# Performance work log

Measured on AMD Instinct MI355X. Metric: run time of the kernel, lower is better.

Reference implementation:

```python
import jax, jax.numpy as jnp
import numpy as np
import math
from jax import lax

PI4 = math.pi / 4.0
BN_EPS = 1e-5


def rotate_kernel(kernel, angle):
    """Bilinear-interpolated rotation of a [Cg, Cg, k, k] kernel by scalar angle."""
    k = kernel.shape[-1]
    c = (k - 1) / 2.0
    cos_t = jnp.cos(angle)
    sin_t = jnp.sin(angle)
    y = jnp.arange(k, dtype=kernel.dtype) - c
    yy, xx = jnp.meshgrid(y, y, indexing='ij')
    x_rot = xx * cos_t + yy * sin_t + c
    y_rot = -xx * sin_t + yy * cos_t + c
    x0 = jnp.clip(jnp.floor(x_rot), 0, k - 2)
    y0 = jnp.clip(jnp.floor(y_rot), 0, k - 2)
    x1 = x0 + 1.0
    y1 = y0 + 1.0
    w00 = (x1 - x_rot) * (y1 - y_rot)
    w01 = (x1 - x_rot) * (y_rot - y0)
    w10 = (x_rot - x0) * (y1 - y_rot)
    w11 = (x_rot - x0) * (y_rot - y0)
    x0i = x0.astype(jnp.int32)
    y0i = y0.astype(jnp.int32)
    x1i = x1.astype(jnp.int32)
    y1i = y1.astype(jnp.int32)
    g = lambda yi, xi: kernel[:, :, yi, xi]  # advanced index -> [Cg,Cg,k,k]
    return w00 * g(y0i, x0i) + w01 * g(y1i, x0i) + w10 * g(y0i, x1i) + w11 * g(y1i, x1i)


def bn_inf(x, w, b, m, v):
    scale = (w / jnp.sqrt(v + BN_EPS))[None, :, None, None]
    return (x - m[None, :, None, None]) * scale + b[None, :, None, None]


def resize_bilinear_ac(x, Ho, Wo):
    """Bilinear resize, align_corners=True, x: [B,C,H,W]."""
    B, C, H, W = x.shape
    ys = jnp.linspace(0.0, H - 1.0, Ho)
    xs = jnp.linspace(0.0, W - 1.0, Wo)
    y0 = jnp.clip(jnp.floor(ys), 0, H - 2).astype(jnp.int32)
    x0 = jnp.clip(jnp.floor(xs), 0, W - 2).astype(jnp.int32)
    wy = (ys - y0)[:, None]
    wx = (xs - x0)[None, :]
    yi0 = y0[:, None]
    xi0 = x0[None, :]
    v00 = x[:, :, yi0, xi0]
    v01 = x[:, :, yi0, xi0 + 1]
    v10 = x[:, :, yi0 + 1, xi0]
    v11 = x[:, :, yi0 + 1, xi0 + 1]
    return (v00 * (1 - wy) * (1 - wx) + v01 * (1 - wy) * wx
            + v10 * wy * (1 - wx) + v11 * wy * wx)


def dac(x, base_kernel, aw1, ab1, aw2, ab2, mw1, mb1, mw2, mb2):
    B, C, H, W = x.shape
    G, Cg = base_kernel.shape[0], base_kernel.shape[1]
    k = base_kernel.shape[-1]
    pad = (k - 1) // 2
    pooled = x.mean(axis=(2, 3))  # [B,C]  (AdaptiveAvgPool2d(1))
    h = jax.nn.relu(pooled @ aw1.T + ab1)
    angles = jnp.tanh(h @ aw2.T + ab2) * PI4  # [B,G]
    # rotate per-(batch, group) kernels: [B,G,Cg,Cg,k,k]
    rot = jax.vmap(lambda ang_b: jax.vmap(rotate_kernel)(base_kernel, ang_b))(angles)
    rhs = rot.reshape(B * C, Cg, k, k)
    # per-sample grouped conv folded into one conv with B*G groups
    feat = lax.conv_general_dilated(
        x.reshape(1, B * C, H, W), rhs, (1, 1), ((pad, pad), (pad, pad)),
        dimension_numbers=('NCHW', 'OIHW', 'NCHW'),
        feature_group_count=B * G).reshape(B, C, H, W)
    mod = jax.nn.sigmoid(jax.nn.relu(pooled @ mw1.T + mb1) @ mw2.T + mb2)  # [B,C]
    return feat * mod[:, :, None, None]


def setup_inputs() -> dict:
    key = jax.random.key(0)
    ks = jax.random.split(key, 32)
    B, C, H, W = 8, 64, 128, 128
    G, Cg, K = 8, 8, 3
    hid = C // 4  # angle/meta hidden = 16
    Ch = C // 2   # edge hidden = 32
    n = lambda i, shape, s: jax.random.normal(ks[i], shape, jnp.float32) * s
    d = {}
    d['x'] = jax.random.normal(ks[0], (B, C, H, W), jnp.float32)
    d['roi_mask'] = jax.random.uniform(ks[1], (B, 1, H // 2, W // 2), jnp.float32)
    # 4 DAC branches stacked on leading axis
    d['base_kernel'] = n(2, (4, G, Cg, Cg, K, K), 0.17)  # kaiming fan_out std
    d['ang_w1'] = n(3, (4, hid, C), 0.1); d['ang_b1'] = n(4, (4, hid), 0.1)
    d['ang_w2'] = n(5, (4, G, hid), 0.1); d['ang_b2'] = n(6, (4, G), 0.1)
    d['meta_w1'] = n(7, (4, hid, C), 0.1); d['meta_b1'] = n(8, (4, hid), 0.1)
    d['meta_w2'] = n(9, (4, C, hid), 0.1); d['meta_b2'] = n(10, (4, C), 0.1)
    # dir_attn: Conv2d_BN(4C->C) + ReLU + Conv(C->4) + Softmax
    d['dir_w1'] = n(11, (C, 4 * C), 0.05)
    d['dir_bn_w'] = jnp.ones((C,), jnp.float32)
    d['dir_bn_b'] = jnp.zeros((C,), jnp.float32)
    d['dir_bn_m'] = n(12, (C,), 0.01)
    d['dir_bn_v'] = jax.random.uniform(ks[13], (C,), jnp.float32, 0.5, 1.5)
    d['dir_w2'] = n(14, (4, C), 0.1); d['dir_b2'] = n(15, (4,), 0.1)
    # edge_attn: Conv2d_BN(C->C/2) + ReLU + Conv(C/2->C) + Sigmoid
    d['edge_w1'] = n(16, (Ch, C), 0.1)
    d['edge_bn_w'] = jnp.ones((Ch,), jnp.float32)
    d['edge_bn_b'] = jnp.zeros((Ch,), jnp.float32)
    d['edge_bn_m'] = n(17, (Ch,), 0.01)
    d['edge_bn_v'] = jax.random.uniform(ks[18], (Ch,), jnp.float32, 0.5, 1.5)
    d['edge_w2'] = n(19, (C, Ch), 0.1); d['edge_b2'] = n(20, (C,), 0.1)
    return d


def reference(x, roi_mask, base_kernel, ang_w1, ang_b1, ang_w2, ang_b2,
              meta_w1, meta_b1, meta_w2, meta_b2,
              dir_w1, dir_bn_w, dir_bn_b, dir_bn_m, dir_bn_v, dir_w2, dir_b2,
              edge_w1, edge_bn_w, edge_bn_b, edge_bn_m, edge_bn_v, edge_w2, edge_b2):
    branch_feats = [
        dac(x, base_kernel[i], ang_w1[i], ang_b1[i], ang_w2[i], ang_b2[i],
            meta_w1[i], meta_b1[i], meta_w2[i], meta_b2[i])
        for i in range(4)
    ]
    feats_cat = jnp.concatenate(branch_feats, axis=1)  # [B,4C,H,W]
    y = jnp.einsum('oc,bchw->bohw', dir_w1, feats_cat)
    y = jax.nn.relu(bn_inf(y, dir_bn_w, dir_bn_b, dir_bn_m, dir_bn_v))
    logits = jnp.einsum('oc,bchw->bohw', dir_w2, y) + dir_b2[None, :, None, None]
    attn = jax.nn.softmax(logits, axis=1)  # [B,4,H,W]
    fused = sum(branch_feats[i] * attn[:, i:i + 1] for i in range(4))
    B, C, H, W = fused.shape
    roi = resize_bilinear_ac(roi_mask, H, W)
    e = jnp.einsum('oc,bchw->bohw', edge_w1, fused * roi)
    e = jax.nn.relu(bn_inf(e, edge_bn_w, edge_bn_b, edge_bn_m, edge_bn_v))
    e = jax.nn.sigmoid(jnp.einsum('oc,bchw->bohw', edge_w2, e) + edge_b2[None, :, None, None])
    return x + x * e
```

## Files before the change

### kernel.cpp

```cpp
#include <hip/hip_runtime.h>
#include <hip/hip_bf16.h>
#include <math.h>

#define PI4F 0.78539816339744830962f

typedef __attribute__((ext_vector_type(2))) __bf16 bf16x2_t;
typedef __attribute__((ext_vector_type(8))) short s8v;
typedef __attribute__((ext_vector_type(4))) float f32x4;
typedef __attribute__((ext_vector_type(4))) unsigned int uint4v;

__device__ __forceinline__ float dot2bf(unsigned int a, unsigned int b, float c) {
#if defined(__has_builtin) && __has_builtin(__builtin_amdgcn_fdot2_f32_bf16)
    return __builtin_amdgcn_fdot2_f32_bf16(__builtin_bit_cast(bf16x2_t, a),
                                           __builtin_bit_cast(bf16x2_t, b), c, false);
#else
    float a0 = __uint_as_float(a << 16), a1 = __uint_as_float(a & 0xffff0000u);
    float b0 = __uint_as_float(b << 16), b1 = __uint_as_float(b & 0xffff0000u);
    return fmaf(a1, b1, fmaf(a0, b0, c));
#endif
}

__device__ __forceinline__ unsigned short bf16bits(float v) {
    return __builtin_bit_cast(unsigned short, __float2bfloat16(v));
}
__device__ __forceinline__ unsigned int packbf(float lo, float hi) {
    return (unsigned int)bf16bits(lo) | ((unsigned int)bf16bits(hi) << 16);
}
__device__ __forceinline__ float ubf_lo(unsigned int u) { return __uint_as_float(u << 16); }
__device__ __forceinline__ float ubf_hi(unsigned int u) { return __uint_as_float(u & 0xffff0000u); }

__global__ void k_pool(const float* __restrict__ x, float* __restrict__ pooled) {
    int bc = blockIdx.x;
    const float4* p4 = (const float4*)(x + (size_t)bc * 16384);
    float s = 0.f;
    for (int j = threadIdx.x; j < 4096; j += 256) {
        float4 v = p4[j];
        s += (v.x + v.y) + (v.z + v.w);
    }
    for (int off = 32; off > 0; off >>= 1) s += __shfl_xor(s, off, 64);
    __shared__ float red[4];
    int wave = threadIdx.x >> 6;
    if ((threadIdx.x & 63) == 0) red[wave] = s;
    __syncthreads();
    if (threadIdx.x == 0) {
        float t = red[0] + red[1] + red[2] + red[3];
        pooled[bc] = t * (1.0f / 16384.0f);
    }
}

__global__ void k_mlp(const float* __restrict__ pooled,
                      const float* __restrict__ aw1, const float* __restrict__ ab1,
                      const float* __restrict__ aw2, const float* __restrict__ ab2,
                      const float* __restrict__ mw1, const float* __restrict__ mb1,
                      const float* __restrict__ mw2, const float* __restrict__ mb2,
                      float* __restrict__ angles, float* __restrict__ mod) {
    int i = blockIdx.x >> 3, b = blockIdx.x & 7;
    int t = threadIdx.x;
    __shared__ float sp[64], sha[16], shm[16];
    sp[t] = pooled[b * 64 + t];
    __syncthreads();
    if (t < 16) {
        float sa = ab1[i * 16 + t], sm = mb1[i * 16 + t];
        const float* wa = aw1 + ((size_t)i * 16 + t) * 64;
        const float* wm = mw1 + ((size_t)i * 16 + t) * 64;
        for (int c = 0; c < 64; ++c) { sa = fmaf(wa[c], sp[c], sa); sm = fmaf(wm[c], sp[c], sm); }
        sha[t] = fmaxf(sa, 0.f);
        shm[t] = fmaxf(sm, 0.f);
    }
    __syncthreads();
    if (t < 8) {
        float s = ab2[i * 8 + t];
        const float* w = aw2 + ((size_t)i * 8 + t) * 16;
        for (int j = 0; j < 16; ++j) s = fmaf(w[j], sha[j], s);
        angles[i * 64 + b * 8 + t] = tanhf(s) * PI4F;
    }
    {
        float s = mb2[i * 64 + t];
        const float* w = mw2 + ((size_t)i * 64 + t) * 16;
        for (int j = 0; j < 16; ++j) s = fmaf(w[j], shm[j], s);
        mod[i * 512 + b * 64 + t] = 1.f / (1.f + expf(-s));
    }
}

__global__ void k_rot(const float* __restrict__ bk, const float* __restrict__ angles,
                      unsigned int* __restrict__ rotp) {
    int blk = blockIdx.x;
    int g = blk & 7, b = (blk >> 3) & 7, i = blk >> 6;
    float ang = angles[i * 64 + b * 8 + g];
    float st, ct;
    sincosf(ang, &st, &ct);
    int t = threadIdx.x;
    int co = t >> 3, ci = t & 7;
    const float* K = bk + ((((size_t)i * 8 + g) * 8 + co) * 8 + ci) * 9;
    __shared__ float tmp[576];
#pragma unroll
    for (int p = 0; p < 9; ++p) {
        int ky = p / 3, kx = p % 3;
        float xx = (float)kx - 1.f, yy = (float)ky - 1.f;
        float xr = xx * ct + yy * st + 1.f;
        float yr = -xx * st + yy * ct + 1.f;
        float x0 = fminf(fmaxf(floorf(xr), 0.f), 1.f);
        float y0 = fminf(fmaxf(floorf(yr), 0.f), 1.f);
        float x1 = x0 + 1.f, y1 = y0 + 1.f;
        float w00 = (x1 - xr) * (y1 - yr);
        float w01 = (x1 - xr) * (yr - y0);
        float w10 = (xr - x0) * (y1 - yr);
        float w11 = (xr - x0) * (yr - y0);
        int x0i = (int)x0, y0i = (int)y0;
        float v = w00 * K[y0i * 3 + x0i] + w01 * K[(y0i + 1) * 3 + x0i]
                + w10 * K[y0i * 3 + x0i + 1] + w11 * K[(y0i + 1) * 3 + x0i + 1];
        tmp[t * 9 + p] = v;
    }
    __syncthreads();
    unsigned int* R = rotp + (size_t)blk * 384;
    for (int ot = t; ot < 384; ot += 64) {
        int co2 = ot / 48;
        int rem = ot - co2 * 48;
        int tap = rem >> 2;
        int q = rem & 3;
        unsigned int val = 0u;
        if (tap < 9) {
            float v0 = tmp[(co2 * 8 + 2 * q) * 9 + tap];
            float v1 = tmp[(co2 * 8 + 2 * q + 1) * 9 + tap];
            val = packbf(v0, v1);
        }
        R[ot] = val;
    }
}

__global__ void k_prep(const float* __restrict__ w1,
                       const float* __restrict__ bnw, const float* __restrict__ bnb,
                       const float* __restrict__ bnm, const float* __restrict__ bnv,
                       const float* __restrict__ ew1,
                       const float* __restrict__ ebnw, const float* __restrict__ ebnb,
                       const float* __restrict__ ebnm, const float* __restrict__ ebnv,
                       const float* __restrict__ ew2,
                       unsigned int* __restrict__ w1f, float* __restrict__ dsh,
                       unsigned int* __restrict__ e1f, float* __restrict__ esh,
                       unsigned int* __restrict__ ew2p) {
    int tid = threadIdx.x;
    __shared__ float sc[64], sce[32];
    if (tid < 64) {
        float s = bnw[tid] * rsqrtf(bnv[tid] + 1e-5f);
        sc[tid] = s;
        dsh[tid] = bnb[tid] - bnm[tid] * s;
    }
    if (tid < 32) {
        float s = ebnw[tid] * rsqrtf(ebnv[tid] + 1e-5f);
        sce[tid] = s;
        esh[tid] = ebnb[tid] - ebnm[tid] * s;
    }
    __syncthreads();
    for (int q = tid; q < 8192; q += 256) {
        int jp = q & 3;
        int l  = (q >> 2) & 63;
        int ks = (q >> 8) & 7;
        int nt = q >> 11;
        int o = nt * 16 + (l & 15);
        int k = ks * 32 + (l >> 4) * 8 + jp * 2;
        w1f[q] = packbf(w1[o * 256 + k] * sc[o], w1[o * 256 + k + 1] * sc[o]);
    }
    for (int q = tid; q < 4096; q += 256) {
        int jp = q & 3;
        int l  = (q >> 2) & 63;
        int kss = (q >> 8) & 1;
        int nt8 = q >> 9;
        int o = (nt8 & 1) * 16 + (l & 15);
        int kloc = kss * 32 + (l >> 4) * 8 + jp * 2;
        e1f[q] = packbf(ew1[o * 64 + kloc] * sce[o], ew1[o * 64 + kloc + 1] * sce[o]);
    }
    for (int q = tid; q < 1024; q += 256) {
        int cc = q >> 4, c2 = q & 15;
        ew2p[q] = packbf(ew2[cc * 32 + 2 * c2], ew2[cc * 32 + 2 * c2 + 1]);
    }
}

__global__ void __launch_bounds__(256) k_conv(const float* __restrict__ x,
                       const unsigned int* __restrict__ rotp, const float* __restrict__ mod,
                       unsigned int* __restrict__ bfu) {
    __shared__ unsigned int s_in[1156 * 6];
    unsigned short* s16 = (unsigned short*)s_in;

    int bg = blockIdx.y;
    int b = bg >> 3, g = bg & 7;
    int tile_h0 = (blockIdx.x >> 2) * 32;
    int tile_w0 = (blockIdx.x & 3) * 32;
    int tid = threadIdx.x;

    const float* xg = x + ((size_t)b * 64 + (size_t)g * 8) * 16384;
    for (int idx = tid; idx < 8 * 1156; idx += 256) {
        int ci = idx / 1156;
        int pix = idx - ci * 1156;
        int r = pix / 34;
        int c = pix - r * 34;
        int gh = tile_h0 + r - 1;
        int gw = tile_w0 + c - 1;
        float v = 0.f;
        if (gh >= 0 && gh < 128 && gw >= 0 && gw < 128)
            v = xg[(size_t)ci * 16384 + gh * 128 + gw];
        s16[pix * 12 + ci] = bf16bits(v);
    }
    __syncthreads();

    int l = tid & 63, wv = tid >> 6;
    int n = l & 15;
    int kg = l >> 4;

    s8v Bf[2][3];
    float mv[2];
#pragma unroll
    for (int bp = 0; bp < 2; ++bp) {
        int i = bp * 2 + (n >> 3);
        int co = n & 7;
        mv[bp] = mod[i * 512 + b * 64 + g * 8 + co];
#pragma unroll
        for (int ks = 0; ks < 3; ++ks) {
            int tap = ks * 4 + kg;
            const uint4v* src = (const uint4v*)(rotp
                + ((size_t)((i * 8 + b) * 8 + g)) * 384 + co * 48 + tap * 4);
            Bf[bp][ks] = __builtin_bit_cast(s8v, *src);
        }
    }

    int hoff6[3];
#pragma unroll
    for (int ks = 0; ks < 3; ++ks) {
        int tap = ks * 4 + kg;
        int t9 = tap > 8 ? 8 : tap;
        int ky = t9 >= 6 ? 2 : (t9 >= 3 ? 1 : 0);
        int kx = t9 - ky * 3;
        hoff6[ks] = (ky * 34 + kx) * 6;
    }

#pragma unroll 2
    for (int t = 0; t < 16; ++t) {
        int px0 = wv * 256 + t * 16;
        int trow = px0 >> 5;
        int tcolb = px0 & 31;
        int basedw = (trow * 34 + tcolb + n) * 6;

        s8v Af[3];
#pragma unroll
        for (int ks = 0; ks < 3; ++ks) {
            const uint2* pa = (const uint2*)(s_in + basedw + hoff6[ks]);
            uint2 v01 = pa[0];
            uint2 v23 = pa[1];
            uint4v au; au.x = v01.x; au.y = v01.y; au.z = v23.x; au.w = v23.y;
            Af[ks] = __builtin_bit_cast(s8v, au);
        }

#pragma unroll
        for (int bp = 0; bp < 2; ++bp) {
            f32x4 acc = (f32x4){0.f, 0.f, 0.f, 0.f};
#pragma unroll
            for (int ks = 0; ks < 3; ++ks)
                acc = __builtin_amdgcn_mfma_f32_16x16x32_bf16(Af[ks], Bf[bp][ks], acc, 0, 0, 0);

            int i = bp * 2 + (n >> 3);
            int co = n & 7;
            float a0 = acc[0] * mv[bp], a1 = acc[1] * mv[bp];
            float a2 = acc[2] * mv[bp], a3 = acc[3] * mv[bp];
            float p0 = __shfl_xor(a0, 1, 64);
            float p1 = __shfl_xor(a1, 1, 64);
            float p2 = __shfl_xor(a2, 1, 64);
            float p3 = __shfl_xor(a3, 1, 64);
            if (!(n & 1)) {
                int pxo = px0 + kg * 4;
                int orow = pxo >> 5, ocol = pxo & 31;
                uint4v st;
                st.x = packbf(a0, p0);
                st.y = packbf(a1, p1);
                st.z = packbf(a2, p2);
                st.w = packbf(a3, p3);
                unsigned int* opu = bfu
                    + (((size_t)(i * 8 + b) * 32) + g * 4 + (co >> 1)) * 16384
                    + (tile_h0 + orow) * 128 + tile_w0 + ocol;
                *(uint4v*)opu = st;
            }
        }
    }
}

__global__ void __launch_bounds__(256, 2) k_mega(
    const float* __restrict__ x, const unsigned int* __restrict__ bfu,
    const float* __restrict__ roi,
    const unsigned int* __restrict__ w1f, const float* __restrict__ dsh,
    const float* __restrict__ w2, const float* __restrict__ b2,
    const unsigned int* __restrict__ e1f, const float* __restrict__ esh,
    const unsigned int* __restrict__ ew2p, const float* __restrict__ eb2,
    float* __restrict__ out) {

    __shared__ unsigned short y_lds[256 * 72];

    int tid = threadIdx.x;
    int p = blockIdx.x * 256 + tid;
    int b = p >> 14;
    int hw = p & 16383;
    int h = hw >> 7, w = hw & 127;
    int hw_base = (blockIdx.x & 63) * 256;

    int l = tid & 63, wv = tid >> 6;
    int arow = l & 15, kg = l >> 4;

    float ysv = (float)h * (63.f / 127.f);
    float y0f = fminf(floorf(ysv), 62.f);
    float wy = ysv - y0f;
    float xsv = (float)w * (63.f / 127.f);
    float x0f = fminf(floorf(xsv), 62.f);
    float wx = xsv - x0f;
    int y0i = (int)y0f, x0i = (int)x0f;
    const float* rb = roi + (size_t)b * 4096;
    float r00 = rb[y0i * 64 + x0i], r01 = rb[y0i * 64 + x0i + 1];
    float r10 = rb[(y0i + 1) * 64 + x0i], r11 = rb[(y0i + 1) * 64 + x0i + 1];
    float rv = r00 * (1.f - wy) * (1.f - wx) + r01 * (1.f - wy) * wx
             + r10 * wy * (1.f - wx) + r11 * wy * wx;

    f32x4 acc[4][4];
#pragma unroll
    for (int mt = 0; mt < 4; ++mt)
#pragma unroll
        for (int nt = 0; nt < 4; ++nt)
            acc[mt][nt] = (f32x4){0.f, 0.f, 0.f, 0.f};
    f32x4 acc2[8][4];
#pragma unroll
    for (int nt8 = 0; nt8 < 8; ++nt8)
#pragma unroll
        for (int mt = 0; mt < 4; ++mt)
            acc2[nt8][mt] = (f32x4){0.f, 0.f, 0.f, 0.f};

#pragma unroll
    for (int ks = 0; ks < 8; ++ks) {
        int k0 = ks * 32 + kg * 8;
        size_t pbase = ((size_t)((k0 >> 6) * 8 + b) * 32 + ((k0 & 63) >> 1)) * 16384;
        s8v af[4];
#pragma unroll
        for (int mt = 0; mt < 4; ++mt) {
            const unsigned int* q = bfu + pbase + hw_base + wv * 64 + mt * 16 + arow;
            uint4v au;
            au.x = q[0];
            au.y = q[16384];
            au.z = q[32768];
            au.w = q[49152];
            af[mt] = __builtin_bit_cast(s8v, au);
        }
        s8v bfr[4];
#pragma unroll
        for (int nt = 0; nt < 4; ++nt) {
            uint4v bu = *(const uint4v*)(w1f + (((nt * 8 + ks) * 64 + l) << 2));
            bfr[nt] = __builtin_bit_cast(s8v, bu);
        }
#pragma unroll
        for (int mt = 0; mt < 4; ++mt)
#pragma unroll
            for (int nt = 0; nt < 4; ++nt)
                acc[mt][nt] = __builtin_amdgcn_mfma_f32_16x16x32_bf16(
                    af[mt], bfr[nt], acc[mt][nt], 0, 0, 0);
        int kss = ks & 1;
#pragma unroll
        for (int t2 = 0; t2 < 2; ++t2) {
            int nt8 = (ks >> 1) * 2 + t2;
            uint4v bu = *(const uint4v*)(e1f + ((nt8 * 2 + kss) * 256 + l * 4));
            s8v bq = __builtin_bit_cast(s8v, bu);
#pragma unroll
            for (int mt = 0; mt < 4; ++mt)
                acc2[nt8][mt] = __builtin_amdgcn_mfma_f32_16x16x32_bf16(
                    af[mt], bq, acc2[nt8][mt], 0, 0, 0);
        }
    }

#pragma unroll
    for (int mt = 0; mt < 4; ++mt)
#pragma unroll
        for (int nt = 0; nt < 4; ++nt)
#pragma unroll
            for (int r = 0; r < 4; ++r) {
                int px = wv * 64 + mt * 16 + kg * 4 + r;
                y_lds[px * 72 + nt * 16 + arow] = bf16bits(acc[mt][nt][r]);
            }
    __syncthreads();

    float y[64];
    {
        const uint4v* yr = (const uint4v*)(y_lds + (size_t)tid * 72);
#pragma unroll
        for (int q8 = 0; q8 < 8; ++q8) {
            uint4v v = yr[q8];
            y[q8 * 8 + 0] = ubf_lo(v.x); y[q8 * 8 + 1] = ubf_hi(v.x);
            y[q8 * 8 + 2] = ubf_lo(v.y); y[q8 * 8 + 3] = ubf_hi(v.y);
            y[q8 * 8 + 4] = ubf_lo(v.z); y[q8 * 8 + 5] = ubf_hi(v.z);
            y[q8 * 8 + 6] = ubf_lo(v.w); y[q8 * 8 + 7] = ubf_hi(v.w);
        }
    }
#pragma unroll
    for (int o = 0; o < 64; ++o) y[o] = fmaxf(y[o] + dsh[o], 0.f);

    float lg[4];
#pragma unroll
    for (int k = 0; k < 4; ++k) {
        float s = b2[k];
        const float* wr = w2 + k * 64;
#pragma unroll
        for (int o = 0; o < 64; ++o) s = fmaf(wr[o], y[o], s);
        lg[k] = s;
    }
    float mx = fmaxf(fmaxf(lg[0], lg[1]), fmaxf(lg[2], lg[3]));
    float e0 = expf(lg[0] - mx), e1s = expf(lg[1] - mx), e2s = expf(lg[2] - mx), e3s = expf(lg[3] - mx);
    float inv = 1.f / (e0 + e1s + e2s + e3s);
    float ar = inv * rv;
    float ar0 = e0 * ar, ar1 = e1s * ar, ar2 = e2s * ar, ar3 = e3s * ar;

    float t[32];
#pragma unroll
    for (int o = 0; o < 32; ++o) t[o] = esh[o];

    __syncthreads();
#pragma unroll
    for (int nt8 = 0; nt8 < 4; ++nt8)
#pragma unroll
        for (int mt = 0; mt < 4; ++mt)
#pragma unroll
            for (int r = 0; r < 4; ++r) {
                int px = wv * 64 + mt * 16 + kg * 4 + r;
                y_lds[px * 72 + nt8 * 16 + arow] = bf16bits(acc2[nt8][mt][r]);
            }
    __syncthreads();
    {
        const uint4v* yr = (const uint4v*)(y_lds + (size_t)tid * 72);
#pragma unroll
        for (int q8 = 0; q8 < 8; ++q8) {
            uint4v v = yr[q8];
            float arq = (q8 < 4) ? ar0 : ar1;
            int base = (q8 & 3) * 8;
            t[base + 0] = fmaf(arq, ubf_lo(v.x), t[base + 0]);
            t[base + 1] = fmaf(arq, ubf_hi(v.x), t[base + 1]);
            t[base + 2] = fmaf(arq, ubf_lo(v.y), t[base + 2]);
            t[base + 3] = fmaf(arq, ubf_hi(v.y), t[base + 3]);
            t[base + 4] = fmaf(arq, ubf_lo(v.z), t[base + 4]);
            t[base + 5] = fmaf(arq, ubf_hi(v.z), t[base + 5]);
            t[base + 6] = fmaf(arq, ubf_lo(v.w), t[base + 6]);
            t[base + 7] = fmaf(arq, ubf_hi(v.w), t[base + 7]);
        }
    }

    __syncthreads();
#pragma unroll
    for (int nt8 = 4; nt8 < 8; ++nt8)
#pragma unroll
        for (int mt = 0; mt < 4; ++mt)
#pragma unroll
            for (int r = 0; r < 4; ++r) {
                int px = wv * 64 + mt * 16 + kg * 4 + r;
                y_lds[px * 72 + (nt8 - 4) * 16 + arow] = bf16bits(acc2[nt8][mt][r]);
            }
    __syncthreads();
    {
        const uint4v* yr = (const uint4v*)(y_lds + (size_t)tid * 72);
#pragma unroll
        for (int q8 = 0; q8 < 8; ++q8) {
            uint4v v = yr[q8];
            float arq = (q8 < 4) ? ar2 : ar3;
            int base = (q8 & 3) * 8;
            t[base + 0] = fmaf(arq, ubf_lo(v.x), t[base + 0]);
            t[base + 1] = fmaf(arq, ubf_hi(v.x), t[base + 1]);
            t[base + 2] = fmaf(arq, ubf_lo(v.y), t[base + 2]);
            t[base + 3] = fmaf(arq, ubf_hi(v.y), t[base + 3]);
            t[base + 4] = fmaf(arq, ubf_lo(v.z), t[base + 4]);
            t[base + 5] = fmaf(arq, ubf_hi(v.z), t[base + 5]);
            t[base + 6] = fmaf(arq, ubf_lo(v.w), t[base + 6]);
            t[base + 7] = fmaf(arq, ubf_hi(v.w), t[base + 7]);
        }
    }

    unsigned int ehp[16];
#pragma unroll
    for (int q = 0; q < 16; ++q)
        ehp[q] = packbf(fmaxf(t[2 * q], 0.f), fmaxf(t[2 * q + 1], 0.f));

    const float* xp = x + ((size_t)b * 64) * 16384 + hw;
    float* op = out + ((size_t)b * 64) * 16384 + hw;
#pragma unroll 8
    for (int cc = 0; cc < 64; ++cc) {
        float s = eb2[cc];
        const unsigned int* wr = ew2p + cc * 16;
#pragma unroll
        for (int q = 0; q < 16; ++q) s = dot2bf(ehp[q], wr[q], s);
        float sg = 1.f / (1.f + expf(-s));
        float xv = xp[(size_t)cc * 16384];
        op[(size_t)cc * 16384] = xv + xv * sg;
    }
}

extern "C" void kernel_launch(void* const* d_in, const int* in_sizes, int n_in,
                              void* d_out, int out_size, void* d_ws, size_t ws_size,
                              hipStream_t stream) {
    const float* x    = (const float*)d_in[0];
    const float* roi  = (const float*)d_in[1];
    const float* bk   = (const float*)d_in[2];
    const float* aw1  = (const float*)d_in[3];
    const float* ab1  = (const float*)d_in[4];
    const float* aw2  = (const float*)d_in[5];
    const float* ab2  = (const float*)d_in[6];
    const float* mw1  = (const float*)d_in[7];
    const float* mb1  = (const float*)d_in[8];
    const float* mw2  = (const float*)d_in[9];
    const float* mb2  = (const float*)d_in[10];
    const float* w1   = (const float*)d_in[11];
    const float* bnw  = (const float*)d_in[12];
    const float* bnb  = (const float*)d_in[13];
    const float* bnm  = (const float*)d_in[14];
    const float* bnv  = (const float*)d_in[15];
    const float* w2   = (const float*)d_in[16];
    const float* b2   = (const float*)d_in[17];
    const float* ew1  = (const float*)d_in[18];
    const float* ebnw = (const float*)d_in[19];
    const float* ebnb = (const float*)d_in[20];
    const float* ebnm = (const float*)d_in[21];
    const float* ebnv = (const float*)d_in[22];
    const float* ew2  = (const float*)d_in[23];
    const float* eb2  = (const float*)d_in[24];

    float* ws     = (float*)d_ws;
    float* pooled = ws;
    float* angles = ws + 512;
    float* mod    = ws + 768;
    unsigned int* rotp = (unsigned int*)(ws + 2816);
    unsigned int* w1f  = (unsigned int*)(ws + 150272);
    float* dsh    = ws + 158464;
    float* esh    = ws + 158528;
    unsigned int* ew2p = (unsigned int*)(ws + 158560);
    unsigned int* e1f  = (unsigned int*)(ws + 159584);
    unsigned int* bfu  = (unsigned int*)(ws + 166720);

    k_prep<<<1, 256, 0, stream>>>(w1, bnw, bnb, bnm, bnv,
                                  ew1, ebnw, ebnb, ebnm, ebnv, ew2,
                                  w1f, dsh, e1f, esh, ew2p);
    k_pool<<<512, 256, 0, stream>>>(x, pooled);
    k_mlp<<<32, 64, 0, stream>>>(pooled, aw1, ab1, aw2, ab2, mw1, mb1, mw2, mb2, angles, mod);
    k_rot<<<256, 64, 0, stream>>>(bk, angles, rotp);
    k_conv<<<dim3(16, 64), 256, 0, stream>>>(x, rotp, mod, bfu);
    k_mega<<<512, 256, 0, stream>>>(x, bfu, roi, w1f, dsh, w2, b2,
                                    e1f, esh, ew2p, eb2,
                                    (float*)d_out);
}
```

Before: 93.69 us.

## Store conv output pixel-major with 8 channels packed per 16-byte word

Changes the intermediate bf16 feature layout from channel-pair planes to per-group planes where each pixel holds all 8 channels of a group contiguously (16 bytes). The conv kernel now transposes its MFMA output across lanes with extra xor shuffles so each lane writes one pixel's 8 channels. The fused kernel can then load each A fragment with a single 16-byte vector load instead of four strided 4-byte loads. The cost is more cross-lane shuffle and select work in the conv epilogue.

```diff
diff --git a/kernel.cpp b/kernel.cpp
--- a/kernel.cpp
+++ b/kernel.cpp
@@ -177,7 +177,7 @@
 
 __global__ void __launch_bounds__(256) k_conv(const float* __restrict__ x,
                        const unsigned int* __restrict__ rotp, const float* __restrict__ mod,
-                       unsigned int* __restrict__ bfu) {
+                       unsigned int* __restrict__ bfq) {
     __shared__ unsigned int s_in[1156 * 6];
     unsigned short* s16 = (unsigned short*)s_in;
 
@@ -205,6 +205,7 @@
     int l = tid & 63, wv = tid >> 6;
     int n = l & 15;
     int kg = l >> 4;
+    int s = (n & 7) >> 1;
 
     s8v Bf[2][3];
     float mv[2];
@@ -257,24 +258,32 @@
                 acc = __builtin_amdgcn_mfma_f32_16x16x32_bf16(Af[ks], Bf[bp][ks], acc, 0, 0, 0);
 
             int i = bp * 2 + (n >> 3);
-            int co = n & 7;
             float a0 = acc[0] * mv[bp], a1 = acc[1] * mv[bp];
             float a2 = acc[2] * mv[bp], a3 = acc[3] * mv[bp];
-            float p0 = __shfl_xor(a0, 1, 64);
-            float p1 = __shfl_xor(a1, 1, 64);
-            float p2 = __shfl_xor(a2, 1, 64);
-            float p3 = __shfl_xor(a3, 1, 64);
+            float q0 = __shfl_xor(a0, 1, 64);
+            float q1 = __shfl_xor(a1, 1, 64);
+            float q2 = __shfl_xor(a2, 1, 64);
+            float q3 = __shfl_xor(a3, 1, 64);
+            unsigned int V0 = packbf(a0, q0), V1 = packbf(a1, q1);
+            unsigned int V2 = packbf(a2, q2), V3 = packbf(a3, q3);
+            unsigned int t0 = __shfl_xor(V0, 2, 64), t1 = __shfl_xor(V1, 2, 64);
+            unsigned int t2 = __shfl_xor(V2, 2, 64), t3 = __shfl_xor(V3, 2, 64);
+            unsigned int U0, U1, U2, U3;
+            if ((s & 1) == 0) { U0 = V0; U1 = t0; U2 = V2; U3 = t2; }
+            else              { U0 = t1; U1 = V1; U2 = t3; U3 = V3; }
+            unsigned int u0 = __shfl_xor(U0, 4, 64), u1 = __shfl_xor(U1, 4, 64);
+            unsigned int u2 = __shfl_xor(U2, 4, 64), u3 = __shfl_xor(U3, 4, 64);
+            unsigned int X0, X1, X2, X3;
+            if ((s & 2) == 0) { X0 = U0; X1 = U1; X2 = u0; X3 = u1; }
+            else              { X0 = u2; X1 = u3; X2 = U2; X3 = U3; }
             if (!(n & 1)) {
-                int pxo = px0 + kg * 4;
+                int pxo = px0 + kg * 4 + s;
                 int orow = pxo >> 5, ocol = pxo & 31;
+                int pixel = (tile_h0 + orow) * 128 + tile_w0 + ocol;
                 uint4v st;
-                st.x = packbf(a0, p0);
-                st.y = packbf(a1, p1);
-                st.z = packbf(a2, p2);
-                st.w = packbf(a3, p3);
-                unsigned int* opu = bfu
-                    + (((size_t)(i * 8 + b) * 32) + g * 4 + (co >> 1)) * 16384
-                    + (tile_h0 + orow) * 128 + tile_w0 + ocol;
+                st.x = X0; st.y = X1; st.z = X2; st.w = X3;
+                unsigned int* opu = bfq
+                    + (((size_t)((i * 8 + b) * 8 + g)) << 16) + ((size_t)pixel << 2);
                 *(uint4v*)opu = st;
             }
         }
@@ -282,7 +291,7 @@
 }
 
 __global__ void __launch_bounds__(256, 2) k_mega(
-    const float* __restrict__ x, const unsigned int* __restrict__ bfu,
+    const float* __restrict__ x, const unsigned int* __restrict__ bfq,
     const float* __restrict__ roi,
     const unsigned int* __restrict__ w1f, const float* __restrict__ dsh,
     const float* __restrict__ w2, const float* __restrict__ b2,
@@ -330,18 +339,15 @@
 
 #pragma unroll
     for (int ks = 0; ks < 8; ++ks) {
-        int k0 = ks * 32 + kg * 8;
-        size_t pbase = ((size_t)((k0 >> 6) * 8 + b) * 32 + ((k0 & 63) >> 1)) * 16384;
+        int i_br = ks >> 1;
+        int grp  = (ks & 1) * 4 + kg;
+        size_t plane = ((size_t)((i_br * 8 + b) * 8 + grp)) << 16;
         s8v af[4];
 #pragma unroll
         for (int mt = 0; mt < 4; ++mt) {
-            const unsigned int* q = bfu + pbase + hw_base + wv * 64 + mt * 16 + arow;
-            uint4v au;
-            au.x = q[0];
-            au.y = q[16384];
-            au.z = q[32768];
-            au.w = q[49152];
-            af[mt] = __builtin_bit_cast(s8v, au);
+            const uint4v* qp = (const uint4v*)(bfq + plane
+                + ((size_t)(hw_base + wv * 64 + mt * 16 + arow) << 2));
+            af[mt] = __builtin_bit_cast(s8v, *qp);
         }
         s8v bfr[4];
 #pragma unroll
@@ -529,7 +535,7 @@
     float* esh    = ws + 158528;
     unsigned int* ew2p = (unsigned int*)(ws + 158560);
     unsigned int* e1f  = (unsigned int*)(ws + 159584);
-    unsigned int* bfu  = (unsigned int*)(ws + 166720);
+    unsigned int* bfq  = (unsigned int*)(ws + 166720);
 
     k_prep<<<1, 256, 0, stream>>>(w1, bnw, bnb, bnm, bnv,
                                   ew1, ebnw, ebnb, ebnm, ebnv, ew2,
@@ -537,8 +543,8 @@
     k_pool<<<512, 256, 0, stream>>>(x, pooled);
     k_mlp<<<32, 64, 0, stream>>>(pooled, aw1, ab1, aw2, ab2, mw1, mb1, mw2, mb2, angles, mod);
     k_rot<<<256, 64, 0, stream>>>(bk, angles, rotp);
-    k_conv<<<dim3(16, 64), 256, 0, stream>>>(x, rotp, mod, bfu);
-    k_mega<<<512, 256, 0, stream>>>(x, bfu, roi, w1f, dsh, w2, b2,
+    k_conv<<<dim3(16, 64), 256, 0, stream>>>(x, rotp, mod, bfq);
+    k_mega<<<512, 256, 0, stream>>>(x, bfq, roi, w1f, dsh, w2, b2,
                                     e1f, esh, ew2p, eb2,
                                     (float*)d_out);
 }
```

New measurement: 105.8 us, median of 3. 12.9% more time.
